# Performance work log

Measured on AMD Instinct MI355X. Metric: run time of the kernel, lower is better.

## Reference

```python
import math
import jax, jax.numpy as jnp
import numpy as np

L, NH, DF = 4, 4, 32  # num_layers, num_heads, head_dim (H=128)
EPS = 1e-5


def ln(x, g, b):
    m = x.mean(-1, keepdims=True)
    v = ((x - m) ** 2).mean(-1, keepdims=True)
    return (x - m) * jax.lax.rsqrt(v + EPS) * g + b


def mha(x, w_in, b_in, w_out, b_out):
    # torch nn.MultiheadAttention self-attention, batch_first, no mask
    B, S, H = x.shape
    q, k, v = jnp.split(x @ w_in + b_in, 3, axis=-1)
    q = q.reshape(B, S, NH, DF)
    k = k.reshape(B, S, NH, DF)
    v = v.reshape(B, S, NH, DF)
    s = jnp.einsum('bqhd,bkhd->bhqk', q, k) / math.sqrt(DF)
    a = jax.nn.softmax(s, axis=-1)
    o = jnp.einsum('bhqk,bkhd->bqhd', a, v).reshape(B, S, H)
    return o @ w_out + b_out


def _forward(X_k, time_embed, step_embed, W_tr, b_tr, W_in, b_in, g_in, be_in,
             W_e, b_e, aw, ab, ow, ob, tng, tnb, f1w, f1b, f2w, f2b, fng, fnb,
             Wq, Wk, Wv, Wo, bo, Wem, bem, Wea, bea, e1w, e1b, e2w, e2b,
             gng, gnb, eng, enb, W_out, b_out, k_index, edge_index):
    B, N, T1, Cin = X_k.shape
    H = W_in.shape[1]
    # --- precompute_graph: self-loops + structural edge features ---
    loop = jnp.arange(N, dtype=edge_index.dtype)
    ei = jnp.concatenate([edge_index, jnp.stack([loop, loop])], axis=1)
    dst, src = ei[0], ei[1]
    E = ei.shape[1]
    deg = jnp.zeros((N,), jnp.float32).at[dst].add(1.0)
    deg_max = jnp.maximum(deg.max(), 1.0)
    edge_w = 1.0 / jnp.maximum(deg[dst], 1.0)
    feat = jnp.stack([edge_w, deg[src] / deg_max, deg[dst] / deg_max], axis=1)  # [E,3]
    # --- input embedding ---
    t_emb = time_embed  # [T1, te] (lookup of arange(T1) = whole table)
    X = jnp.concatenate(
        [X_k, jnp.broadcast_to(t_emb[None, None], (B, N, T1, t_emb.shape[-1]))], axis=-1)
    h = ln(X @ W_in + b_in, g_in, be_in)
    h = h + step_embed[k_index][:, None, None, :]
    e = feat @ W_e + b_e                       # [E, de]
    t_re = t_emb @ W_tr + b_tr                 # [T1, H]
    BT = B * T1
    for l in range(L):
        # temporal attention over T1
        h_flat = h.reshape(B * N, T1, H)
        attn_out = mha(h_flat, aw[l], ab[l], ow[l], ob[l])
        h = ln(h + attn_out.reshape(B, N, T1, H), tng[l], tnb[l])
        ffn = jax.nn.gelu(h @ f1w[l] + f1b[l], approximate=False) @ f2w[l] + f2b[l]
        h = ln(h + ffn, fng[l], fnb[l])
        h = h + t_re[None, None]
        # DiGress GT sparse graph block over N
        h_BT = h.transpose(0, 2, 1, 3).reshape(BT, N, H)
        Q = (h_BT @ Wq[l]).reshape(BT, N, NH, DF)
        K = (h_BT @ Wk[l]).reshape(BT, N, NH, DF)
        V = (h_BT @ Wv[l]).reshape(BT, N, NH, DF)
        scores = (Q[:, dst] * K[:, src]).sum(-1) / math.sqrt(DF)  # [BT,E,NH]
        scores = scores * (e @ Wem[l] + bem[l] + 1.0) + (e @ Wea[l] + bea[l])
        s_max = jax.lax.stop_gradient(scores.max(axis=1, keepdims=True))
        exp_s = jnp.exp(scores - s_max)
        denom = jnp.zeros((BT, N, NH), exp_s.dtype).at[:, dst, :].add(exp_s)
        attn = exp_s / (denom[:, dst, :] + 1e-9)
        agg = (attn[..., None] * V[:, src]).reshape(BT, E, H)
        out = jnp.zeros((BT, N, H), h.dtype).at[:, dst, :].add(agg)
        h_BT = h_BT + out @ Wo[l] + bo[l]
        h_mean = jax.lax.stop_gradient(h_BT).mean(0)               # [N,H]
        e_in = jnp.concatenate([h_mean[dst], h_mean[src], e], axis=-1)
        e_mlp = jax.nn.gelu(e_in @ e1w[l] + e1b[l], approximate=False) @ e2w[l] + e2b[l]
        e = ln(e + e_mlp, eng[l], enb[l])
        h = ln(h_BT.reshape(B, T1, N, H).transpose(0, 2, 1, 3), gng[l], gnb[l])
    return jax.nn.softmax(h @ W_out + b_out, axis=-1)


def setup_inputs() -> dict:
    key = jax.random.key(0)
    B, N, T1 = 2, 2000, 12
    sd, cc, te, H, de, nh = 4, 2, 16, 128, 16, 4
    Cin = (1 + cc) * sd  # 12
    E0, max_steps = 32000, 1024
    ks = iter(jax.random.split(key, 60))
    def rn(*shape, s=0.05):
        return jax.random.normal(next(ks), shape, jnp.float32) * s
    z = lambda *s: jnp.zeros(s, jnp.float32)
    o = lambda *s: jnp.ones(s, jnp.float32)
    return dict(
        X_k=jax.random.normal(next(ks), (B, N, T1, Cin), jnp.float32),
        time_embed=rn(T1, te), step_embed=rn(max_steps, H),
        W_tr=rn(te, H), b_tr=z(H),
        W_in=rn(Cin + te, H), b_in=z(H), g_in=o(H), be_in=z(H),
        W_e=rn(3, de), b_e=z(de),
        aw=rn(L, H, 3 * H), ab=z(L, 3 * H), ow=rn(L, H, H), ob=z(L, H),
        tng=o(L, H), tnb=z(L, H),
        f1w=rn(L, H, 2 * H), f1b=z(L, 2 * H), f2w=rn(L, 2 * H, H), f2b=z(L, H),
        fng=o(L, H), fnb=z(L, H),
        Wq=rn(L, H, H), Wk=rn(L, H, H), Wv=rn(L, H, H),
        Wo=rn(L, H, H), bo=z(L, H),
        Wem=rn(L, de, nh), bem=z(L, nh), Wea=rn(L, de, nh), bea=z(L, nh),
        e1w=rn(L, 2 * H + de, 4 * de), e1b=z(L, 4 * de),
        e2w=rn(L, 4 * de, de), e2b=z(L, de),
        gng=o(L, H), gnb=z(L, H), eng=o(L, de), enb=z(L, de),
        W_out=rn(H, sd), b_out=z(sd),
        k_index=jax.random.randint(next(ks), (B,), 0, max_steps),
        edge_index=jax.random.randint(next(ks), (2, E0), 0, N),
    )


def reference(X_k, time_embed, step_embed, W_tr, b_tr, W_in, b_in, g_in, be_in,
              W_e, b_e, aw, ab, ow, ob, tng, tnb, f1w, f1b, f2w, f2b, fng, fnb,
              Wq, Wk, Wv, Wo, bo, Wem, bem, Wea, bea, e1w, e1b, e2w, e2b,
              gng, gnb, eng, enb, W_out, b_out, k_index, edge_index):
    return _forward(X_k, time_embed, step_embed, W_tr, b_tr, W_in, b_in, g_in, be_in,
                    W_e, b_e, aw, ab, ow, ob, tng, tnb, f1w, f1b, f2w, f2b, fng, fnb,
                    Wq, Wk, Wv, Wo, bo, Wem, bem, Wea, bea, e1w, e1b, e2w, e2b,
                    gng, gnb, eng, enb, W_out, b_out, k_index, edge_index)
```

## Files before the change

### kernel.cpp

```cpp
#include <hip/hip_runtime.h>
#include <math.h>

#define NN 2000
#define T1C 12
#define BBC 2
#define HHC 128
#define NHD 4
#define DFD 32
#define LLC 4
#define DEC 16
#define TEC 16
#define CINC 12
#define E0C 32000
#define EEC 34000
#define BTC 24
#define MROWS 48000
#define EPSLN 1e-5f
#define SCALEQK 0.17677669529663687f

typedef __attribute__((ext_vector_type(8))) short short8;
typedef __attribute__((ext_vector_type(4))) float f32x4;


__device__ __forceinline__ unsigned short f2b(float f)
{
    unsigned u = __float_as_uint(f);
    return (unsigned short)((u + 0x7FFF + ((u >> 16) & 1)) >> 16);
}

__device__ __forceinline__ float b2f(unsigned short h)
{
    return __uint_as_float(((unsigned)h) << 16);
}


__global__ __launch_bounds__(256) void convwp_k(const float* __restrict__ W, unsigned short* __restrict__ Bp,
                                                int LN_, int K, int N, int noff, int Ntot)
{
    int idx = blockIdx.x * blockDim.x + threadIdx.x;
    int total = LN_ * K * N;
    if (idx >= total) return;
    int l = idx / (K * N);
    int r = idx - l * (K * N);
    int k = r / N;
    int n = r - k * N + noff;
    size_t off = (size_t)l * K * Ntot +
                 ((size_t)((n >> 4) * (K >> 5) + (k >> 5)) << 9) +
                 (((k >> 3) & 3) << 7) + ((n & 15) << 3) + (k & 7);
    Bp[off] = f2b(W[idx]);
}

__global__ __launch_bounds__(256) void convw12_k(const float* __restrict__ e1w, unsigned short* __restrict__ W12P)
{
    int idx = blockIdx.x * blockDim.x + threadIdx.x;
    if (idx >= LLC * 128 * 128) return;
    int l = idx >> 14;
    int r = idx & 16383;
    int c = r >> 7, k = r & 127;
    int sk = (c < 64) ? k : k + 128;
    int sc = c & 63;
    W12P[idx] = f2b(e1w[((size_t)l * 272 + sk) * 64 + sc]);
}

__global__ __launch_bounds__(256) void convwoT_k(const float* __restrict__ Wo, unsigned short* __restrict__ WoT)
{
    int idx = blockIdx.x * blockDim.x + threadIdx.x;
    if (idx >= LLC * 128 * 128) return;
    int l = idx >> 14;
    int r = idx & 16383;
    int c = r >> 7, k = r & 127;
    WoT[idx] = f2b(Wo[((size_t)l * 128 + k) * 128 + c]);
}


template<int K, int EPI, int OUTM>
__global__ __launch_bounds__(256) void gemm2_k(
    const unsigned short* __restrict__ A, const unsigned short* __restrict__ Bp,
    const float* __restrict__ bias, float* __restrict__ C, unsigned short* __restrict__ Cb,
    const float* __restrict__ res, const float* __restrict__ gam, const float* __restrict__ bet,
    const float* __restrict__ trep,
    int M, int Ntot)
{
    __shared__ unsigned short A_s[128 * 16 * 8];
    __shared__ float red2[2][128][2];

    int tid = threadIdx.x;
    int w = tid >> 6, lane = tid & 63;
    int wr = w & 1, wc = w >> 1;
    int quad = lane >> 4, lr = lane & 15;

    const unsigned short* abase = A + (size_t)blockIdx.x * 128 * K;
    int ntg0 = blockIdx.y * 8 + wc * 4;

    f32x4 acc[4][4];
#pragma unroll
    for (int mt = 0; mt < 4; mt++)
#pragma unroll
        for (int nt = 0; nt < 4; nt++) acc[mt][nt] = (f32x4){0.f, 0.f, 0.f, 0.f};

#pragma unroll
    for (int kb = 0; kb < K; kb += 128) {
        if (kb) __syncthreads();
#pragma unroll
        for (int j = 0; j < 8; j++) {
            int s = j * 256 + tid;
            int row = s >> 4, ks = s & 15;
            int ko = ks ^ (row & 15);
            uint4 d = *(const uint4*)(abase + (size_t)row * K + kb + ko * 8);
            *(uint4*)(A_s + s * 8) = d;
        }
        __syncthreads();
#pragma unroll
        for (int k0 = 0; k0 < 128; k0 += 32) {
            short8 af[4], bf[4];
#pragma unroll
            for (int mt = 0; mt < 4; mt++) {
                int row_l = wr * 64 + mt * 16 + lr;
                int koct = (k0 >> 3) + quad;
                int slot = row_l * 16 + (koct ^ lr);
                af[mt] = *(const short8*)(A_s + slot * 8);
            }
#pragma unroll
            for (int nt = 0; nt < 4; nt++) {
                size_t off = ((size_t)(ntg0 + nt) * (K >> 5) + ((kb + k0) >> 5)) * 512 + lane * 8;
                bf[nt] = *(const short8*)(Bp + off);
            }
#pragma unroll
            for (int mt = 0; mt < 4; mt++)
#pragma unroll
                for (int nt = 0; nt < 4; nt++)
                    acc[mt][nt] = __builtin_amdgcn_mfma_f32_16x16x32_bf16(af[mt], bf[nt], acc[mt][nt], 0, 0, 0);
        }
    }

    int rbase = blockIdx.x * 128 + wr * 64;
    int cbase = blockIdx.y * 128 + wc * 64;

    if constexpr (EPI != 3 && EPI != 4 && EPI != 5) {
#pragma unroll
        for (int mt = 0; mt < 4; mt++) {
#pragma unroll
            for (int nt = 0; nt < 4; nt++) {
                int colg = cbase + nt * 16 + lr;
                float bv = bias ? bias[colg] : 0.f;
#pragma unroll
                for (int i = 0; i < 4; i++) {
                    int row = rbase + mt * 16 + quad * 4 + i;
                    float x = acc[mt][nt][i] + bv;
                    if constexpr (EPI == 1) x = 0.5f * x * (1.f + erff(x * 0.70710678118654752f));
                    if constexpr (EPI == 2) x = res[(size_t)row * Ntot + colg] + x;
                    if constexpr (OUTM & 1) C[(size_t)row * Ntot + colg] = x;
                    if constexpr (OUTM & 4)
                        Cb[(size_t)blockIdx.y * M * 128 + (size_t)row * 128 + (wc * 64 + nt * 16 + lr)] = f2b(x);
                    else if constexpr (OUTM & 2)
                        Cb[(size_t)row * Ntot + colg] = f2b(x);
                }
            }
        }
    } else {
        float s[4][4], s2l[4][4];
#pragma unroll
        for (int mt = 0; mt < 4; mt++)
#pragma unroll
            for (int i = 0; i < 4; i++) { s[mt][i] = 0.f; s2l[mt][i] = 0.f; }
#pragma unroll
        for (int mt = 0; mt < 4; mt++) {
#pragma unroll
            for (int nt = 0; nt < 4; nt++) {
                int colg = cbase + nt * 16 + lr;
                float bv = bias[colg];
#pragma unroll
                for (int i = 0; i < 4; i++) {
                    int row = rbase + mt * 16 + quad * 4 + i;
                    float x = acc[mt][nt][i] + bv + res[(size_t)row * 128 + colg];
                    acc[mt][nt][i] = x;
                    s[mt][i] += x;
                    s2l[mt][i] += x * x;
                }
            }
        }
#pragma unroll
        for (int m = 1; m < 16; m <<= 1) {
#pragma unroll
            for (int mt = 0; mt < 4; mt++)
#pragma unroll
                for (int i = 0; i < 4; i++) {
                    s[mt][i]  += __shfl_xor(s[mt][i], m, 64);
                    s2l[mt][i] += __shfl_xor(s2l[mt][i], m, 64);
                }
        }
        if (lr == 0) {
#pragma unroll
            for (int mt = 0; mt < 4; mt++)
#pragma unroll
                for (int i = 0; i < 4; i++) {
                    int rl = wr * 64 + mt * 16 + quad * 4 + i;
                    red2[wc][rl][0] = s[mt][i];
                    red2[wc][rl][1] = s2l[mt][i];
                }
        }
        __syncthreads();
#pragma unroll
        for (int mt = 0; mt < 4; mt++) {
#pragma unroll
            for (int i = 0; i < 4; i++) {
                int rl = wr * 64 + mt * 16 + quad * 4 + i;
                float st  = red2[0][rl][0] + red2[1][rl][0];
                float s2t = red2[0][rl][1] + red2[1][rl][1];
                float mu = st * (1.f / 128.f);
                float rstd = rsqrtf(s2t * (1.f / 128.f) - mu * mu + EPSLN);
                int row = rbase + mt * 16 + quad * 4 + i;
                if constexpr (EPI == 4) {
                    int t = row % T1C;
                    int bn = row / T1C;
                    int b = bn / NN;
                    int n = bn - b * NN;
                    size_t rowp = (size_t)(b * T1C + t) * NN + n;
                    const float* trow = trep + t * HHC;
#pragma unroll
                    for (int nt = 0; nt < 4; nt++) {
                        int colg = cbase + nt * 16 + lr;
                        float y = (acc[mt][nt][i] - mu) * rstd * gam[colg] + bet[colg] + trow[colg];
                        C[rowp * 128 + colg] = y;
                        Cb[rowp * 128 + colg] = f2b(y);
                    }
                } else if constexpr (EPI == 5) {
                    int bt = row / NN, n = row - bt * NN;
                    int b = bt / T1C, t = bt - b * T1C;
                    size_t rowp = ((size_t)(b * NN + n)) * T1C + t;
#pragma unroll
                    for (int nt = 0; nt < 4; nt++) {
                        int colg = cbase + nt * 16 + lr;
                        float y = (acc[mt][nt][i] - mu) * rstd * gam[colg] + bet[colg];
                        C[rowp * 128 + colg] = y;
                        Cb[rowp * 128 + colg] = f2b(y);
                    }
                } else {
#pragma unroll
                    for (int nt = 0; nt < 4; nt++) {
                        int colg = cbase + nt * 16 + lr;
                        float y = (acc[mt][nt][i] - mu) * rstd * gam[colg] + bet[colg];
                        if constexpr (OUTM & 1) C[(size_t)row * 128 + colg] = y;
                        if constexpr (OUTM & 2) Cb[(size_t)row * 128 + colg] = f2b(y);
                    }
                }
            }
        }
    }
}

template<int K, int EPI, int OUTM>
static void run_gemm2(const unsigned short* A, const unsigned short* Bp, const float* bias,
                      float* C, unsigned short* Cb, const float* res, const float* g, const float* be,
                      const float* trep, int M, int Ntot, hipStream_t stream)
{
    dim3 grid(M / 128, Ntot / 128);
    gemm2_k<K, EPI, OUTM><<<grid, 256, 0, stream>>>(A, Bp, bias, C, Cb, res, g, be, trep, M, Ntot);
}


__global__ __launch_bounds__(256) void offn_k(
    const unsigned short* __restrict__ A,
    const unsigned short* __restrict__ Wp,
    const float* __restrict__ ob_l,
    const float* __restrict__ resh,
    const float* __restrict__ tng_l, const float* __restrict__ tnb_l,
    const unsigned short* __restrict__ F1p,
    const unsigned short* __restrict__ F2p,
    const float* __restrict__ f1b_l, const float* __restrict__ f2b_l,
    const float* __restrict__ fng_l, const float* __restrict__ fnb_l,
    const float* __restrict__ trep,
    const unsigned short* __restrict__ Wqkv,
    float* __restrict__ C,
    unsigned short* __restrict__ Qc, unsigned short* __restrict__ Kc, unsigned short* __restrict__ Vc)
{
    __shared__ unsigned short A_s[32 * 16 * 8];
    __shared__ unsigned short M_s[32 * 16 * 8];
    __shared__ float red2[2][32][2];

    int tid = threadIdx.x;
    int w = tid >> 6, lane = tid & 63;
    int wr = w & 1, wc = w >> 1;
    int quad = lane >> 4, lr = lane & 15;

    const unsigned short* abase = A + (size_t)blockIdx.x * 32 * 128;

#pragma unroll
    for (int j = 0; j < 2; j++) {
        int s = j * 256 + tid;
        int row = s >> 4, ks = s & 15;
        int ko = ks ^ (row & 15);
        uint4 d = *(const uint4*)(abase + (size_t)row * 128 + ko * 8);
        *(uint4*)(A_s + s * 8) = d;
    }
    __syncthreads();

    f32x4 wacc[4];
#pragma unroll
    for (int nt = 0; nt < 4; nt++) wacc[nt] = (f32x4){0.f, 0.f, 0.f, 0.f};
#pragma unroll
    for (int k0 = 0; k0 < 128; k0 += 32) {
        int row_l = wr * 16 + lr;
        int koct = (k0 >> 3) + quad;
        int slot = row_l * 16 + (koct ^ lr);
        short8 af = *(const short8*)(A_s + slot * 8);
        short8 bf[4];
#pragma unroll
        for (int nt = 0; nt < 4; nt++) {
            size_t off = ((size_t)(wc * 4 + nt) * 4 + (k0 >> 5)) * 512 + lane * 8;
            bf[nt] = *(const short8*)(Wp + off);
        }
#pragma unroll
        for (int nt = 0; nt < 4; nt++)
            wacc[nt] = __builtin_amdgcn_mfma_f32_16x16x32_bf16(af, bf[nt], wacc[nt], 0, 0, 0);
    }

    int rbase = blockIdx.x * 32 + wr * 16;
    int cbase = wc * 64;

    float yv[4][4];
    {
        float s1[4], s2v[4];
#pragma unroll
        for (int i = 0; i < 4; i++) { s1[i] = 0.f; s2v[i] = 0.f; }
#pragma unroll
        for (int nt = 0; nt < 4; nt++) {
            int colg = cbase + nt * 16 + lr;
            float bv = ob_l[colg];
#pragma unroll
            for (int i = 0; i < 4; i++) {
                int row = rbase + quad * 4 + i;
                float x = wacc[nt][i] + bv + resh[(size_t)row * 128 + colg];
                yv[nt][i] = x;
                s1[i] += x;
                s2v[i] += x * x;
            }
        }
#pragma unroll
        for (int m = 1; m < 16; m <<= 1) {
#pragma unroll
            for (int i = 0; i < 4; i++) {
                s1[i]  += __shfl_xor(s1[i], m, 64);
                s2v[i] += __shfl_xor(s2v[i], m, 64);
            }
        }
        if (lr == 0) {
#pragma unroll
            for (int i = 0; i < 4; i++) {
                int rl = wr * 16 + quad * 4 + i;
                red2[wc][rl][0] = s1[i];
                red2[wc][rl][1] = s2v[i];
            }
        }
        __syncthreads();
#pragma unroll
        for (int i = 0; i < 4; i++) {
            int rl = wr * 16 + quad * 4 + i;
            float st  = red2[0][rl][0] + red2[1][rl][0];
            float s2t = red2[0][rl][1] + red2[1][rl][1];
            float mu = st * (1.f / 128.f);
            float rstd = rsqrtf(s2t * (1.f / 128.f) - mu * mu + EPSLN);
            int row = wr * 16 + quad * 4 + i;
#pragma unroll
            for (int nt = 0; nt < 4; nt++) {
                int col = cbase + nt * 16 + lr;
                float y = (yv[nt][i] - mu) * rstd * tng_l[col] + tnb_l[col];
                yv[nt][i] = y;
                int cchunk = col >> 3, celem = col & 7;
                int ks = cchunk ^ (row & 15);
                A_s[(row * 16 + ks) * 8 + celem] = f2b(y);
            }
        }
    }
    __syncthreads();

    f32x4 facc[4];
#pragma unroll
    for (int nt = 0; nt < 4; nt++) facc[nt] = (f32x4){0.f, 0.f, 0.f, 0.f};

#pragma unroll
    for (int half = 0; half < 2; half++) {
        f32x4 macc[4];
#pragma unroll
        for (int nt = 0; nt < 4; nt++) macc[nt] = (f32x4){0.f, 0.f, 0.f, 0.f};
#pragma unroll
        for (int k0 = 0; k0 < 128; k0 += 32) {
            int row_l = wr * 16 + lr;
            int koct = (k0 >> 3) + quad;
            int slot = row_l * 16 + (koct ^ lr);
            short8 af = *(const short8*)(A_s + slot * 8);
            short8 bf[4];
#pragma unroll
            for (int nt = 0; nt < 4; nt++) {
                size_t off = ((size_t)(half * 8 + wc * 4 + nt) * 4 + (k0 >> 5)) * 512 + lane * 8;
                bf[nt] = *(const short8*)(F1p + off);
            }
#pragma unroll
            for (int nt = 0; nt < 4; nt++)
                macc[nt] = __builtin_amdgcn_mfma_f32_16x16x32_bf16(af, bf[nt], macc[nt], 0, 0, 0);
        }
        if (half) __syncthreads();
#pragma unroll
        for (int nt = 0; nt < 4; nt++) {
            int col = wc * 64 + nt * 16 + lr;
            float bv = f1b_l[half * 128 + col];
            int cchunk = col >> 3, celem = col & 7;
#pragma unroll
            for (int i = 0; i < 4; i++) {
                int row = wr * 16 + quad * 4 + i;
                float x = macc[nt][i] + bv;
                x = 0.5f * x * (1.f + erff(x * 0.70710678118654752f));
                int ks = cchunk ^ (row & 15);
                M_s[(row * 16 + ks) * 8 + celem] = f2b(x);
            }
        }
        __syncthreads();
#pragma unroll
        for (int k0 = 0; k0 < 128; k0 += 32) {
            int row_l = wr * 16 + lr;
            int koct = (k0 >> 3) + quad;
            int slot = row_l * 16 + (koct ^ lr);
            short8 af = *(const short8*)(M_s + slot * 8);
            short8 bf[4];
#pragma unroll
            for (int nt = 0; nt < 4; nt++) {
                size_t off = ((size_t)(wc * 4 + nt) * 8 + ((half * 128 + k0) >> 5)) * 512 + lane * 8;
                bf[nt] = *(const short8*)(F2p + off);
            }
#pragma unroll
            for (int nt = 0; nt < 4; nt++)
                facc[nt] = __builtin_amdgcn_mfma_f32_16x16x32_bf16(af, bf[nt], facc[nt], 0, 0, 0);
        }
    }

    float s[4], s2l[4];
#pragma unroll
    for (int i = 0; i < 4; i++) { s[i] = 0.f; s2l[i] = 0.f; }
#pragma unroll
    for (int nt = 0; nt < 4; nt++) {
        int colg = cbase + nt * 16 + lr;
        float bv = f2b_l[colg];
#pragma unroll
        for (int i = 0; i < 4; i++) {
            float x = facc[nt][i] + bv + yv[nt][i];
            facc[nt][i] = x;
            s[i] += x;
            s2l[i] += x * x;
        }
    }
#pragma unroll
    for (int m = 1; m < 16; m <<= 1) {
#pragma unroll
        for (int i = 0; i < 4; i++) {
            s[i]  += __shfl_xor(s[i], m, 64);
            s2l[i] += __shfl_xor(s2l[i], m, 64);
        }
    }
    if (lr == 0) {
#pragma unroll
        for (int i = 0; i < 4; i++) {
            int rl = wr * 16 + quad * 4 + i;
            red2[wc][rl][0] = s[i];
            red2[wc][rl][1] = s2l[i];
        }
    }
    __syncthreads();
    size_t rowp4[4];
#pragma unroll
    for (int i = 0; i < 4; i++) {
        int rl = wr * 16 + quad * 4 + i;
        float st  = red2[0][rl][0] + red2[1][rl][0];
        float s2t = red2[0][rl][1] + red2[1][rl][1];
        float mu = st * (1.f / 128.f);
        float rstd = rsqrtf(s2t * (1.f / 128.f) - mu * mu + EPSLN);
        int row = rbase + quad * 4 + i;
        int t = row % T1C;
        int bn = row / T1C;
        int b = bn / NN;
        int n = bn - b * NN;
        size_t rowp = (size_t)(b * T1C + t) * NN + n;
        rowp4[i] = rowp;
        const float* trow = trep + t * HHC;
        int rloc = wr * 16 + quad * 4 + i;
#pragma unroll
        for (int nt = 0; nt < 4; nt++) {
            int colg = cbase + nt * 16 + lr;
            float y = (facc[nt][i] - mu) * rstd * fng_l[colg] + fnb_l[colg] + trow[colg];
            C[rowp * 128 + colg] = y;
            int cchunk = colg >> 3, celem = colg & 7;
            int ks = cchunk ^ (rloc & 15);
            A_s[(rloc * 16 + ks) * 8 + celem] = f2b(y);
        }
    }
    __syncthreads();

#pragma unroll
    for (int g3 = 0; g3 < 3; g3++) {
        f32x4 qacc[4];
#pragma unroll
        for (int nt = 0; nt < 4; nt++) qacc[nt] = (f32x4){0.f, 0.f, 0.f, 0.f};
#pragma unroll
        for (int k0 = 0; k0 < 128; k0 += 32) {
            int row_l = wr * 16 + lr;
            int koct = (k0 >> 3) + quad;
            int slot = row_l * 16 + (koct ^ lr);
            short8 af = *(const short8*)(A_s + slot * 8);
            short8 bf[4];
#pragma unroll
            for (int nt = 0; nt < 4; nt++) {
                size_t off = ((size_t)(wc * 12 + g3 * 4 + nt) * 4 + (k0 >> 5)) * 512 + lane * 8;
                bf[nt] = *(const short8*)(Wqkv + off);
            }
#pragma unroll
            for (int nt = 0; nt < 4; nt++)
                qacc[nt] = __builtin_amdgcn_mfma_f32_16x16x32_bf16(af, bf[nt], qacc[nt], 0, 0, 0);
        }
#pragma unroll
        for (int nt = 0; nt < 4; nt++) {
            int colg = wc * 192 + (g3 * 4 + nt) * 16 + lr;
            unsigned short* dstbuf;
            int col;
            if (colg < 128)      { dstbuf = Qc; col = colg; }
            else if (colg < 256) { dstbuf = Kc; col = colg - 128; }
            else                 { dstbuf = Vc; col = colg - 256; }
#pragma unroll
            for (int i = 0; i < 4; i++)
                dstbuf[rowp4[i] * 128 + col] = f2b(qacc[nt][i]);
        }
    }
}


__global__ __launch_bounds__(256) void gemm_hm12_k(
    const unsigned short* __restrict__ A,
    const unsigned short* __restrict__ WT,
    const float* __restrict__ mA, const float* __restrict__ bo,
    const unsigned short* __restrict__ W12,
    float* __restrict__ P12)
{
    __shared__ unsigned short A_s[32 * 16 * 8];
    const int M = NN, K = 128;
    int tid = threadIdx.x;
    int w = tid >> 6, lane = tid & 63;
    int wr = w & 1, wc = w >> 1;
    int r0 = blockIdx.x * 32 + wr * 16;
    int c0 = wc * 64;
    int lr = lane & 15, quad = lane >> 4;
    int kq = quad * 8;
    int arow = r0 + lr; if (arow >= M) arow = M - 1;
    const unsigned short* ap = A + (size_t)arow * K + kq;
    const unsigned short* wp = WT + (size_t)(c0 + lr) * K + kq;

    f32x4 acc[4];
#pragma unroll
    for (int t = 0; t < 4; t++) acc[t] = (f32x4){0.f, 0.f, 0.f, 0.f};
    for (int k0 = 0; k0 < K; k0 += 32) {
        short8 a = *(const short8*)(ap + k0);
#pragma unroll
        for (int t = 0; t < 4; t++) {
            short8 b = *(const short8*)(wp + (size_t)t * 16 * K + k0);
            acc[t] = __builtin_amdgcn_mfma_f32_16x16x32_bf16(a, b, acc[t], 0, 0, 0);
        }
    }
#pragma unroll
    for (int t = 0; t < 4; t++) {
        int col = c0 + t * 16 + lr;
        int cchunk = col >> 3, celem = col & 7;
#pragma unroll
        for (int i = 0; i < 4; i++) {
            int row = r0 + quad * 4 + i;
            int rr = row < M ? row : M - 1;
            float x = acc[t][i] + mA[(size_t)rr * 128 + col] + bo[col];
            int rloc = wr * 16 + quad * 4 + i;
            int ks = cchunk ^ (rloc & 15);
            A_s[(rloc * 16 + ks) * 8 + celem] = f2b(x);
        }
    }
    __syncthreads();

    f32x4 acc2[4];
#pragma unroll
    for (int t = 0; t < 4; t++) acc2[t] = (f32x4){0.f, 0.f, 0.f, 0.f};
    const unsigned short* wp2 = W12 + (size_t)(c0 + lr) * 128 + kq;
#pragma unroll
    for (int k0 = 0; k0 < 128; k0 += 32) {
        int row_l = wr * 16 + lr;
        int koct = (k0 >> 3) + quad;
        int slot = row_l * 16 + (koct ^ lr);
        short8 af = *(const short8*)(A_s + slot * 8);
#pragma unroll
        for (int t = 0; t < 4; t++) {
            short8 b = *(const short8*)(wp2 + (size_t)t * 16 * 128 + k0);
            acc2[t] = __builtin_amdgcn_mfma_f32_16x16x32_bf16(af, b, acc2[t], 0, 0, 0);
        }
    }
#pragma unroll
    for (int t = 0; t < 4; t++) {
        int col = c0 + t * 16 + lr;
#pragma unroll
        for (int i = 0; i < 4; i++) {
            int row = r0 + quad * 4 + i;
            if (row < M) P12[(size_t)row * 128 + col] = acc2[t][i];
        }
    }
}


__global__ __launch_bounds__(256) void emlp_k(const float* __restrict__ P12,
                                              const int* __restrict__ dst, const int* __restrict__ src,
                                              const float* __restrict__ e1wE, const float* __restrict__ e1b_l,
                                              const float* __restrict__ e2w_l, const float* __restrict__ e2b_l,
                                              const float* __restrict__ g, const float* __restrict__ be,
                                              float* __restrict__ e,
                                              const int* __restrict__ epos,
                                              const float* __restrict__ WemN, const float* __restrict__ bemN,
                                              const float* __restrict__ WeaN, const float* __restrict__ beaN,
                                              float* __restrict__ ec, int doEc)
{
    __shared__ float tl[4][64];
    int wv = threadIdx.x >> 6, l = threadIdx.x & 63;
    int r = blockIdx.x * 4 + wv;
    int d = dst[r], s = src[r];
    const float* ep = e + (size_t)r * DEC;
    float t = P12[(size_t)d * 128 + l] + P12[(size_t)s * 128 + 64 + l] + e1b_l[l];
#pragma unroll
    for (int k = 0; k < DEC; k++) t += ep[k] * e1wE[k * 64 + l];
    t = 0.5f * t * (1.f + erff(t * 0.70710678118654752f));
    tl[wv][l] = t;
    __syncthreads();
    int c = l & 15, kq = l >> 4;
    float p = 0.f;
#pragma unroll
    for (int j = 0; j < 16; j++) p += tl[wv][kq * 16 + j] * e2w_l[(kq * 16 + j) * 16 + c];
    p += __shfl_xor(p, 16, 64);
    p += __shfl_xor(p, 32, 64);
    float x = p + e2b_l[c] + ep[c];
    float s1 = x, s2 = x * x;
#pragma unroll
    for (int m = 1; m < 16; m <<= 1) {
        s1 += __shfl_xor(s1, m, 64);
        s2 += __shfl_xor(s2, m, 64);
    }
    float mu = s1 * (1.f / 16.f);
    float rstd = rsqrtf(s2 * (1.f / 16.f) - mu * mu + EPSLN);
    float y = (x - mu) * rstd * g[c] + be[c];
    if (l < 16) e[(size_t)r * DEC + c] = y;

    if (doEc) {
        int hh = l >> 4;
        float pem = y * WemN[c * NHD + hh];
        float pea = y * WeaN[c * NHD + hh];
#pragma unroll
        for (int m = 1; m < 16; m <<= 1) {
            pem += __shfl_xor(pem, m, 64);
            pea += __shfl_xor(pea, m, 64);
        }
        if (c == 0) {
            int pos = epos[r];
            ec[(size_t)pos * 8 + hh * 2]     = (pem + bemN[hh] + 1.f) * SCALEQK;
            ec[(size_t)pos * 8 + hh * 2 + 1] = pea + beaN[hh];
        }
    }
}


__global__ __launch_bounds__(256) void zero_deg_k(int* __restrict__ degi)
{
    int i = blockIdx.x * blockDim.x + threadIdx.x;
    if (i < NN) degi[i] = 0;
}

__global__ __launch_bounds__(256) void build_edges_k(const int* __restrict__ eidx,
                                                     int* __restrict__ dst, int* __restrict__ src,
                                                     int* __restrict__ degi)
{
    int e = blockIdx.x * blockDim.x + threadIdx.x;
    if (e >= EEC) return;
    int d, s;
    if (e < E0C) { d = eidx[e]; s = eidx[E0C + e]; }
    else { d = e - E0C; s = e - E0C; }
    dst[e] = d;
    src[e] = s;
    atomicAdd(&degi[d], 1);
}

__global__ __launch_bounds__(256) void scan_k(const int* __restrict__ degi, int* __restrict__ rowptr,
                                              int* __restrict__ cursor, float* __restrict__ degmaxf)
{
    __shared__ int ssum[256];
    __shared__ int smx[256];
    int tid = threadIdx.x;
    int vals[8];
    int s = 0, mx = 0;
    int base = tid * 8;
#pragma unroll
    for (int j = 0; j < 8; j++) {
        int idx = base + j;
        int v = (idx < NN) ? degi[idx] : 0;
        vals[j] = v; s += v; mx = max(mx, v);
    }
    ssum[tid] = s; smx[tid] = mx;
    __syncthreads();
    for (int off = 1; off < 256; off <<= 1) {
        int t = (tid >= off) ? ssum[tid - off] : 0;
        __syncthreads();
        ssum[tid] += t;
        __syncthreads();
    }
    for (int off = 128; off > 0; off >>= 1) {
        if (tid < off) smx[tid] = max(smx[tid], smx[tid + off]);
        __syncthreads();
    }
    if (tid == 0) *degmaxf = fmaxf((float)smx[0], 1.f);
    int running = ssum[tid] - s;
#pragma unroll
    for (int j = 0; j < 8; j++) {
        int idx = base + j;
        if (idx < NN) { rowptr[idx] = running; cursor[idx] = running; running += vals[j]; }
    }
    if (tid == 255) rowptr[NN] = ssum[255];
}

__global__ __launch_bounds__(256) void feat_k(const int* __restrict__ dst, const int* __restrict__ src,
                                              const int* __restrict__ degi, const float* __restrict__ degmaxf,
                                              int* __restrict__ cursor, int* __restrict__ srcCSR,
                                              int* __restrict__ epos,
                                              const float* __restrict__ We, const float* __restrict__ bE,
                                              float* __restrict__ e)
{
    int ei = blockIdx.x * blockDim.x + threadIdx.x;
    if (ei >= EEC) return;
    int d = dst[ei], s = src[ei];
    int pos = atomicAdd(&cursor[d], 1);
    srcCSR[pos] = s;
    epos[ei] = pos;
    float dm = *degmaxf;
    float degd = (float)degi[d], degs = (float)degi[s];
    float f0 = 1.f / fmaxf(degd, 1.f);
    float f1 = degs / dm, f2 = degd / dm;
#pragma unroll
    for (int c = 0; c < DEC; c++)
        e[ei * DEC + c] = bE[c] + f0 * We[c] + f1 * We[DEC + c] + f2 * We[2 * DEC + c];
}


__global__ __launch_bounds__(256) void embed_k(const float* __restrict__ Xk, const float* __restrict__ temb,
                                               const float* __restrict__ Win, const float* __restrict__ bin,
                                               const float* __restrict__ g, const float* __restrict__ be,
                                               const float* __restrict__ stepemb, const int* __restrict__ kidx,
                                               float* __restrict__ h, unsigned short* __restrict__ hb)
{
    int row = blockIdx.x * 4 + (threadIdx.x >> 6);
    int l = threadIdx.x & 63;
    int t = row % T1C;
    int bn = row / T1C;
    int b = bn / NN;
    const float* xk = Xk + (size_t)row * CINC;
    const float* tp = temb + t * TEC;
    float acc0 = bin[l], acc1 = bin[l + 64];
#pragma unroll
    for (int k = 0; k < CINC; k++) {
        float xv = xk[k];
        acc0 += xv * Win[k * HHC + l];
        acc1 += xv * Win[k * HHC + l + 64];
    }
#pragma unroll
    for (int k = 0; k < TEC; k++) {
        float xv = tp[k];
        acc0 += xv * Win[(CINC + k) * HHC + l];
        acc1 += xv * Win[(CINC + k) * HHC + l + 64];
    }
    float s = acc0 + acc1, s2 = acc0 * acc0 + acc1 * acc1;
#pragma unroll
    for (int m = 32; m >= 1; m >>= 1) {
        s  += __shfl_xor(s, m, 64);
        s2 += __shfl_xor(s2, m, 64);
    }
    float mu = s * (1.f / 128.f);
    float rstd = rsqrtf(s2 * (1.f / 128.f) - mu * mu + EPSLN);
    const float* se = stepemb + (size_t)kidx[b] * HHC;
    float v0 = (acc0 - mu) * rstd * g[l] + be[l] + se[l];
    float v1 = (acc1 - mu) * rstd * g[l + 64] + be[l + 64] + se[l + 64];
    size_t ob = (size_t)row * HHC;
    h[ob + l] = v0;
    h[ob + l + 64] = v1;
    hb[ob + l] = f2b(v0);
    hb[ob + l + 64] = f2b(v1);
}

__global__ __launch_bounds__(128) void tre_k(const float* __restrict__ temb, const float* __restrict__ Wtr,
                                             const float* __restrict__ btr, float* __restrict__ tre)
{
    int t = blockIdx.x, c = threadIdx.x;
    float acc = btr[c];
#pragma unroll
    for (int k = 0; k < TEC; k++) acc += temb[t * TEC + k] * Wtr[k * HHC + c];
    tre[t * HHC + c] = acc;
}


__global__ __launch_bounds__(128) void temporal_attn_k(const unsigned short* __restrict__ qkvb,
                                                       unsigned short* __restrict__ outb)
{
    int bn = blockIdx.x;
    __shared__ unsigned short qkv_s[T1C][408];
    __shared__ float s[NHD][T1C][T1C];
    int tid = threadIdx.x;
    int hh = tid >> 5, lane = tid & 31;
    const unsigned short* base = qkvb + (size_t)bn * T1C * 384;
    for (int cIdx = tid; cIdx < 576; cIdx += 128) {
        uint4 d = *(const uint4*)(base + cIdx * 8);
        int t = cIdx / 48;
        int c0 = (cIdx - t * 48) * 8;
        *(uint4*)(&qkv_s[t][c0]) = d;
    }
    __syncthreads();
    for (int idx = lane; idx < T1C * T1C; idx += 32) {
        int tq = idx / T1C, tk = idx - tq * T1C;
        const unsigned* qp = (const unsigned*)&qkv_s[tq][hh * 32];
        const unsigned* kp = (const unsigned*)&qkv_s[tk][128 + hh * 32];
        float acc = 0.f;
#pragma unroll
        for (int d = 0; d < 16; d++) {
            unsigned a = qp[d], b = kp[d];
            acc += __uint_as_float(a << 16) * __uint_as_float(b << 16);
            acc += __uint_as_float(a & 0xFFFF0000u) * __uint_as_float(b & 0xFFFF0000u);
        }
        s[hh][tq][tk] = acc * SCALEQK;
    }
    __syncthreads();
    if (tid < NHD * T1C) {
        int h2 = tid / T1C, tq = tid - h2 * T1C;
        float mx = -1e30f;
#pragma unroll
        for (int j = 0; j < T1C; j++) mx = fmaxf(mx, s[h2][tq][j]);
        float sum = 0.f;
#pragma unroll
        for (int j = 0; j < T1C; j++) { float ex = __expf(s[h2][tq][j] - mx); s[h2][tq][j] = ex; sum += ex; }
        float inv = 1.f / sum;
#pragma unroll
        for (int j = 0; j < T1C; j++) s[h2][tq][j] *= inv;
    }
    __syncthreads();
    int oc = hh * 32 + lane;
#pragma unroll
    for (int t = 0; t < T1C; t++) {
        float acc = 0.f;
#pragma unroll
        for (int tk = 0; tk < T1C; tk++) acc += s[hh][t][tk] * b2f(qkv_s[tk][256 + oc]);
        outb[((size_t)bn * T1C + t) * HHC + oc] = f2b(acc);
    }
}


__global__ __launch_bounds__(256) void emea_k(const float* __restrict__ e, const int* __restrict__ epos,
                                              const float* __restrict__ Wem, const float* __restrict__ bem,
                                              const float* __restrict__ Wea, const float* __restrict__ bea,
                                              float* __restrict__ ec)
{
    int r = blockIdx.x * blockDim.x + threadIdx.x;
    if (r >= EEC) return;
    float ev[DEC];
#pragma unroll
    for (int k = 0; k < DEC; k++) ev[k] = e[r * DEC + k];
    int pos = epos[r];
#pragma unroll
    for (int hh = 0; hh < NHD; hh++) {
        float a = bem[hh], b2 = bea[hh];
#pragma unroll
        for (int k = 0; k < DEC; k++) { a += ev[k] * Wem[k * NHD + hh]; b2 += ev[k] * Wea[k * NHD + hh]; }
        ec[(size_t)pos * 8 + hh * 2]     = (a + 1.f) * SCALEQK;
        ec[(size_t)pos * 8 + hh * 2 + 1] = b2;
    }
}

__global__ __launch_bounds__(256) void sagg_k(const unsigned short* __restrict__ Q,
                                              const unsigned short* __restrict__ K,
                                              const unsigned short* __restrict__ V,
                                              const int* __restrict__ rowptr, const int* __restrict__ srcCSR,
                                              const float* __restrict__ ec, unsigned short* __restrict__ outb)
{
    int wv = threadIdx.x >> 6;
    int lane = threadIdx.x & 63;
    int blk = blockIdx.x;
    int bt = blk % BTC;
    int n  = (blk / BTC) * 4 + wv;
    int cg = lane & 15;
    int es = lane >> 4;
    int hh = cg >> 2;
    size_t base = (size_t)bt * NN;
    uint4 qd = *(const uint4*)(Q + (base + n) * HHC + cg * 8);
    unsigned qv[4] = {qd.x, qd.y, qd.z, qd.w};
    float q[8];
#pragma unroll
    for (int jj = 0; jj < 4; jj++) {
        q[2 * jj]     = __uint_as_float(qv[jj] << 16);
        q[2 * jj + 1] = __uint_as_float(qv[jj] & 0xFFFF0000u);
    }
    int s0 = rowptr[n], s1 = rowptr[n + 1];
    float acc[8];
#pragma unroll
    for (int j = 0; j < 8; j++) acc[j] = 0.f;
    float den = 0.f;
    for (int i = s0 + es; i < s1; i += 4) {
        int sn = srcCSR[i];
        uint4 kd = *(const uint4*)(K + (base + sn) * HHC + cg * 8);
        uint4 vd = *(const uint4*)(V + (base + sn) * HHC + cg * 8);
        float2 c2 = *(const float2*)(ec + (size_t)i * 8 + hh * 2);
        unsigned kv[4] = {kd.x, kd.y, kd.z, kd.w};
        float p = 0.f;
#pragma unroll
        for (int jj = 0; jj < 4; jj++) {
            p += q[2 * jj]     * __uint_as_float(kv[jj] << 16);
            p += q[2 * jj + 1] * __uint_as_float(kv[jj] & 0xFFFF0000u);
        }
        p += __shfl_xor(p, 1, 64);
        p += __shfl_xor(p, 2, 64);
        float w = __expf(p * c2.x + c2.y);
        unsigned vv[4] = {vd.x, vd.y, vd.z, vd.w};
#pragma unroll
        for (int jj = 0; jj < 4; jj++) {
            acc[2 * jj]     += w * __uint_as_float(vv[jj] << 16);
            acc[2 * jj + 1] += w * __uint_as_float(vv[jj] & 0xFFFF0000u);
        }
        den += w;
    }
#pragma unroll
    for (int j = 0; j < 8; j++) {
        acc[j] += __shfl_xor(acc[j], 16, 64);
        acc[j] += __shfl_xor(acc[j], 32, 64);
    }
    den += __shfl_xor(den, 16, 64);
    den += __shfl_xor(den, 32, 64);
    if (es == 0) {
        float inv = den + 1e-9f;
        unsigned short r[8];
#pragma unroll
        for (int j = 0; j < 8; j++) r[j] = f2b(acc[j] / inv);
        *(uint4*)(outb + (base + n) * HHC + cg * 8) = *(uint4*)r;
    }
}

__global__ __launch_bounds__(128) void hmean2_k(const float* __restrict__ hBT,
                                                const unsigned short* __restrict__ aggb,
                                                float* __restrict__ mA, unsigned short* __restrict__ mBb)
{
    int n = blockIdx.x, c = threadIdx.x;
    float sA = 0.f, sB = 0.f;
#pragma unroll
    for (int bt = 0; bt < BTC; bt++) {
        size_t off = ((size_t)bt * NN + n) * HHC + c;
        sA += hBT[off];
        sB += b2f(aggb[off]);
    }
    mA[n * HHC + c] = sA * (1.f / BTC);
    mBb[n * HHC + c] = f2b(sB * (1.f / BTC));
}


__global__ __launch_bounds__(256) void out_k(const float* __restrict__ h, const float* __restrict__ Wout,
                                             const float* __restrict__ bout, float* __restrict__ out)
{
    int row = blockIdx.x * 4 + (threadIdx.x >> 6);
    int lane = threadIdx.x & 63;
    const float* hp = h + (size_t)row * HHC;
    float x0 = hp[lane], x1 = hp[lane + 64];
    float w00 = Wout[lane * 4 + 0], w01 = Wout[lane * 4 + 1];
    float w02 = Wout[lane * 4 + 2], w03 = Wout[lane * 4 + 3];
    float w10 = Wout[(lane + 64) * 4 + 0], w11 = Wout[(lane + 64) * 4 + 1];
    float w12 = Wout[(lane + 64) * 4 + 2], w13 = Wout[(lane + 64) * 4 + 3];
    float p0 = x0 * w00 + x1 * w10;
    float p1 = x0 * w01 + x1 * w11;
    float p2 = x0 * w02 + x1 * w12;
    float p3 = x0 * w03 + x1 * w13;
#pragma unroll
    for (int m = 32; m >= 1; m >>= 1) {
        p0 += __shfl_xor(p0, m, 64);
        p1 += __shfl_xor(p1, m, 64);
        p2 += __shfl_xor(p2, m, 64);
        p3 += __shfl_xor(p3, m, 64);
    }
    if (lane == 0) {
        float l0 = p0 + bout[0], l1 = p1 + bout[1], l2 = p2 + bout[2], l3 = p3 + bout[3];
        float mx = fmaxf(fmaxf(l0, l1), fmaxf(l2, l3));
        float e0 = __expf(l0 - mx), e1 = __expf(l1 - mx), e2 = __expf(l2 - mx), e3 = __expf(l3 - mx);
        float inv = 1.f / (e0 + e1 + e2 + e3);
        float4 o = {e0 * inv, e1 * inv, e2 * inv, e3 * inv};
        *(float4*)(out + (size_t)row * 4) = o;
    }
}


extern "C" void kernel_launch(void* const* d_in, const int* in_sizes, int n_in,
                              void* d_out, int out_size, void* d_ws, size_t ws_size,
                              hipStream_t stream)
{
    const float* Xk      = (const float*)d_in[0];
    const float* temb    = (const float*)d_in[1];
    const float* stepemb = (const float*)d_in[2];
    const float* Wtr     = (const float*)d_in[3];
    const float* btr     = (const float*)d_in[4];
    const float* Win     = (const float*)d_in[5];
    const float* bin     = (const float*)d_in[6];
    const float* gin     = (const float*)d_in[7];
    const float* bein    = (const float*)d_in[8];
    const float* We      = (const float*)d_in[9];
    const float* bE      = (const float*)d_in[10];
    const float* aw      = (const float*)d_in[11];
    const float* ab      = (const float*)d_in[12];
    const float* ow      = (const float*)d_in[13];
    const float* ob      = (const float*)d_in[14];
    const float* tng     = (const float*)d_in[15];
    const float* tnb     = (const float*)d_in[16];
    const float* f1w     = (const float*)d_in[17];
    const float* f1b     = (const float*)d_in[18];
    const float* f2w     = (const float*)d_in[19];
    const float* f2b_    = (const float*)d_in[20];
    const float* fng     = (const float*)d_in[21];
    const float* fnb     = (const float*)d_in[22];
    const float* Wq      = (const float*)d_in[23];
    const float* Wk      = (const float*)d_in[24];
    const float* Wv      = (const float*)d_in[25];
    const float* Wo      = (const float*)d_in[26];
    const float* bo      = (const float*)d_in[27];
    const float* Wem     = (const float*)d_in[28];
    const float* bem     = (const float*)d_in[29];
    const float* Wea     = (const float*)d_in[30];
    const float* bea     = (const float*)d_in[31];
    const float* e1w     = (const float*)d_in[32];
    const float* e1b     = (const float*)d_in[33];
    const float* e2w     = (const float*)d_in[34];
    const float* e2b     = (const float*)d_in[35];
    const float* gng     = (const float*)d_in[36];
    const float* gnb     = (const float*)d_in[37];
    const float* eng     = (const float*)d_in[38];
    const float* enb     = (const float*)d_in[39];
    const float* Wout    = (const float*)d_in[40];
    const float* bout    = (const float*)d_in[41];
    const int*   kidx    = (const int*)d_in[42];
    const int*   eidx    = (const int*)d_in[43];
    float* outp = (float*)d_out;

    char* wsp = (char*)d_ws;
    auto alloc = [&](size_t nbytes) -> void* {
        void* p = (void*)wsp;
        wsp += (nbytes + 255) & ~(size_t)255;
        return p;
    };
    float* h     = (float*)alloc((size_t)MROWS * HHC * 4);
    unsigned short* hb = (unsigned short*)alloc((size_t)MROWS * HHC * 2);
    float* hBT   = (float*)alloc((size_t)MROWS * HHC * 4);
    float* bufC  = (float*)alloc((size_t)MROWS * 384 * 4);
    unsigned short* bufDb = (unsigned short*)alloc((size_t)MROWS * HHC * 2);
    float* ebuf  = (float*)alloc((size_t)EEC * DEC * 4);
    float* ec    = (float*)alloc((size_t)EEC * NHD * 2 * 4);
    float* P12   = (float*)alloc((size_t)NN * HHC * 4);
    float* mA    = (float*)alloc((size_t)NN * HHC * 4);
    unsigned short* mBb = (unsigned short*)alloc((size_t)NN * HHC * 2);
    float* tre   = (float*)alloc((size_t)T1C * HHC * 4);
    float* degmaxf = (float*)alloc(4);
    int* degi   = (int*)alloc((size_t)NN * 4);
    int* dst    = (int*)alloc((size_t)EEC * 4);
    int* srcA   = (int*)alloc((size_t)EEC * 4);
    int* srcCSR = (int*)alloc((size_t)EEC * 4);
    int* epos   = (int*)alloc((size_t)EEC * 4);
    int* rowptr = (int*)alloc((size_t)(NN + 1) * 4);
    int* cursor = (int*)alloc((size_t)NN * 4);
    unsigned short* awP   = (unsigned short*)alloc((size_t)LLC * 384 * 128 * 2);
    unsigned short* owP   = (unsigned short*)alloc((size_t)LLC * 128 * 128 * 2);
    unsigned short* f1P   = (unsigned short*)alloc((size_t)LLC * 256 * 128 * 2);
    unsigned short* f2P   = (unsigned short*)alloc((size_t)LLC * 128 * 256 * 2);
    unsigned short* WqkvP = (unsigned short*)alloc((size_t)LLC * 384 * 128 * 2);
    unsigned short* WoP   = (unsigned short*)alloc((size_t)LLC * 128 * 128 * 2);
    unsigned short* WoT   = (unsigned short*)alloc((size_t)LLC * 128 * 128 * 2);
    unsigned short* W12P  = (unsigned short*)alloc((size_t)LLC * 128 * 128 * 2);

    unsigned short* bufCb = (unsigned short*)bufC;
    unsigned short* Qc    = (unsigned short*)bufC;
    unsigned short* Kc    = Qc + (size_t)MROWS * HHC;
    unsigned short* Vc    = Kc + (size_t)MROWS * HHC;

    {
        auto cwp = [&](const float* W, unsigned short* Bp, int K, int N, int noff, int Ntot) {
            int total = LLC * K * N;
            convwp_k<<<(total + 255) / 256, 256, 0, stream>>>(W, Bp, LLC, K, N, noff, Ntot);
        };
        cwp(aw,  awP, 128, 384, 0, 384);
        cwp(ow,  owP, 128, 128, 0, 128);
        cwp(f1w, f1P, 128, 256, 0, 256);
        cwp(f2w, f2P, 256, 128, 0, 128);
        cwp(Wq,  WqkvP, 128, 128, 0,   384);
        cwp(Wk,  WqkvP, 128, 128, 128, 384);
        cwp(Wv,  WqkvP, 128, 128, 256, 384);
        cwp(Wo,  WoP, 128, 128, 0, 128);
        convwoT_k<<<(LLC * 128 * 128 + 255) / 256, 256, 0, stream>>>(Wo, WoT);
        convw12_k<<<(LLC * 128 * 128 + 255) / 256, 256, 0, stream>>>(e1w, W12P);
    }

    zero_deg_k<<<(NN + 255) / 256, 256, 0, stream>>>(degi);
    build_edges_k<<<(EEC + 255) / 256, 256, 0, stream>>>(eidx, dst, srcA, degi);
    scan_k<<<1, 256, 0, stream>>>(degi, rowptr, cursor, degmaxf);
    feat_k<<<(EEC + 255) / 256, 256, 0, stream>>>(dst, srcA, degi, degmaxf, cursor, srcCSR, epos, We, bE, ebuf);

    embed_k<<<MROWS / 4, 256, 0, stream>>>(Xk, temb, Win, bin, gin, bein, stepemb, kidx, h, hb);
    tre_k<<<T1C, 128, 0, stream>>>(temb, Wtr, btr, tre);

    emea_k<<<(EEC + 255) / 256, 256, 0, stream>>>(ebuf, epos, Wem, bem, Wea, bea, ec);

    for (int l = 0; l < LLC; l++) {
        const unsigned short* awP_l   = awP   + (size_t)l * 384 * 128;
        const unsigned short* owP_l   = owP   + (size_t)l * 128 * 128;
        const unsigned short* f1P_l   = f1P   + (size_t)l * 256 * 128;
        const unsigned short* f2P_l   = f2P   + (size_t)l * 128 * 256;
        const unsigned short* WqkvP_l = WqkvP + (size_t)l * 384 * 128;
        const unsigned short* WoP_l   = WoP   + (size_t)l * 128 * 128;
        const unsigned short* WoT_l   = WoT   + (size_t)l * 128 * 128;
        const unsigned short* W12P_l  = W12P  + (size_t)l * 128 * 128;
        const float* ab_l  = ab  + (size_t)l * 3 * HHC;
        const float* ob_l  = ob  + (size_t)l * HHC;
        const float* tng_l = tng + (size_t)l * HHC;
        const float* tnb_l = tnb + (size_t)l * HHC;
        const float* f1b_l = f1b + (size_t)l * 256;
        const float* f2b_l = f2b_ + (size_t)l * HHC;
        const float* fng_l = fng + (size_t)l * HHC;
        const float* fnb_l = fnb + (size_t)l * HHC;
        const float* bo_l  = bo  + (size_t)l * HHC;
        const float* e1wE_l = e1w + ((size_t)l * 272 + 256) * 64;
        const float* e1b_l = e1b + (size_t)l * 64;
        const float* e2w_l = e2w + (size_t)l * 64 * DEC;
        const float* e2b_l = e2b + (size_t)l * DEC;
        const float* gng_l = gng + (size_t)l * HHC;
        const float* gnb_l = gnb + (size_t)l * HHC;
        const float* eng_l = eng + (size_t)l * DEC;
        const float* enb_l = enb + (size_t)l * DEC;
        int ln = (l + 1 < LLC) ? l + 1 : l;
        const float* WemN = Wem + (size_t)ln * DEC * NHD;
        const float* bemN = bem + (size_t)ln * NHD;
        const float* WeaN = Wea + (size_t)ln * DEC * NHD;
        const float* beaN = bea + (size_t)ln * NHD;
        int doEc = (l + 1 < LLC) ? 1 : 0;

        run_gemm2<128, 0, 2>(hb, awP_l, ab_l, nullptr, bufCb, nullptr, nullptr, nullptr, nullptr, MROWS, 384, stream);
        temporal_attn_k<<<BBC * NN, 128, 0, stream>>>(bufCb, bufDb);
        offn_k<<<MROWS / 32, 256, 0, stream>>>(bufDb, owP_l, ob_l, h, tng_l, tnb_l,
                                               f1P_l, f2P_l, f1b_l, f2b_l, fng_l, fnb_l,
                                               tre, WqkvP_l, hBT, Qc, Kc, Vc);
        sagg_k<<<BTC * (NN / 4), 256, 0, stream>>>(Qc, Kc, Vc, rowptr, srcCSR, ec, bufDb);
        hmean2_k<<<NN, 128, 0, stream>>>(hBT, bufDb, mA, mBb);
        run_gemm2<128, 5, 3>(bufDb, WoP_l, bo_l, h, hb, hBT, gng_l, gnb_l, nullptr, MROWS, 128, stream);
        gemm_hm12_k<<<(NN + 31) / 32, 256, 0, stream>>>(mBb, WoT_l, mA, bo_l, W12P_l, P12);
        emlp_k<<<EEC / 4, 256, 0, stream>>>(P12, dst, srcA, e1wE_l, e1b_l, e2w_l, e2b_l, eng_l, enb_l, ebuf,
                                            epos, WemN, bemN, WeaN, beaN, ec, doEc);
    }

    out_k<<<MROWS / 4, 256, 0, stream>>>(h, Wout, bout, outp);
}
```

Measured before the change: 933.3 us.

## Fuse next layer's QKV projection into the LayerNorm epilogue of the output GEMM

The spatial output GEMM with its LayerNorm epilogue now also keeps the normalized bf16 tile in shared memory and runs the next layer's QKV projection on it, writing Q/K/V straight into bufCb in permuted row order. The standalone QKV GEMM in each layer is removed, except for a single launch before the loop for layer 0. This drops one kernel launch per layer and the write and re-read of the bf16 hidden copy (hb). In exchange the fused kernel does three times more MFMA work per block while its grid stays at 375 blocks, which may serialise work that used to be spread over 1125 blocks.

```diff
diff --git a/kernel.cpp b/kernel.cpp
--- a/kernel.cpp
+++ b/kernel.cpp
@@ -73,16 +73,19 @@
 }
 
 
-template<int K, int EPI, int OUTM>
+template<int K, int EPI, int OUTM, int QKV>
 __global__ __launch_bounds__(256) void gemm2_k(
     const unsigned short* __restrict__ A, const unsigned short* __restrict__ Bp,
     const float* __restrict__ bias, float* __restrict__ C, unsigned short* __restrict__ Cb,
     const float* __restrict__ res, const float* __restrict__ gam, const float* __restrict__ bet,
     const float* __restrict__ trep,
+    const unsigned short* __restrict__ Wqkv, const float* __restrict__ abq,
+    unsigned short* __restrict__ outQ,
     int M, int Ntot)
 {
     __shared__ unsigned short A_s[128 * 16 * 8];
     __shared__ float red2[2][128][2];
+    __shared__ int rowp_s[128];
 
     int tid = threadIdx.x;
     int w = tid >> 6, lane = tid & 63;
@@ -136,7 +139,7 @@
     int rbase = blockIdx.x * 128 + wr * 64;
     int cbase = blockIdx.y * 128 + wc * 64;
 
-    if constexpr (EPI != 3 && EPI != 4 && EPI != 5) {
+    if constexpr (EPI != 3 && EPI != 5) {
 #pragma unroll
         for (int mt = 0; mt < 4; mt++) {
 #pragma unroll
@@ -150,10 +153,7 @@
                     if constexpr (EPI == 1) x = 0.5f * x * (1.f + erff(x * 0.70710678118654752f));
                     if constexpr (EPI == 2) x = res[(size_t)row * Ntot + colg] + x;
                     if constexpr (OUTM & 1) C[(size_t)row * Ntot + colg] = x;
-                    if constexpr (OUTM & 4)
-                        Cb[(size_t)blockIdx.y * M * 128 + (size_t)row * 128 + (wc * 64 + nt * 16 + lr)] = f2b(x);
-                    else if constexpr (OUTM & 2)
-                        Cb[(size_t)row * Ntot + colg] = f2b(x);
+                    if constexpr (OUTM & 2) Cb[(size_t)row * Ntot + colg] = f2b(x);
                 }
             }
         }
@@ -210,30 +210,22 @@
                 float mu = st * (1.f / 128.f);
                 float rstd = rsqrtf(s2t * (1.f / 128.f) - mu * mu + EPSLN);
                 int row = rbase + mt * 16 + quad * 4 + i;
-                if constexpr (EPI == 4) {
-                    int t = row % T1C;
-                    int bn = row / T1C;
-                    int b = bn / NN;
-                    int n = bn - b * NN;
-                    size_t rowp = (size_t)(b * T1C + t) * NN + n;
-                    const float* trow = trep + t * HHC;
-#pragma unroll
-                    for (int nt = 0; nt < 4; nt++) {
-                        int colg = cbase + nt * 16 + lr;
-                        float y = (acc[mt][nt][i] - mu) * rstd * gam[colg] + bet[colg] + trow[colg];
-                        C[rowp * 128 + colg] = y;
-                        Cb[rowp * 128 + colg] = f2b(y);
-                    }
-                } else if constexpr (EPI == 5) {
+                if constexpr (EPI == 5) {
                     int bt = row / NN, n = row - bt * NN;
                     int b = bt / T1C, t = bt - b * T1C;
                     size_t rowp = ((size_t)(b * NN + n)) * T1C + t;
+                    if (QKV && lr == 0) rowp_s[rl] = (int)rowp;
 #pragma unroll
                     for (int nt = 0; nt < 4; nt++) {
                         int colg = cbase + nt * 16 + lr;
                         float y = (acc[mt][nt][i] - mu) * rstd * gam[colg] + bet[colg];
                         C[rowp * 128 + colg] = y;
-                        Cb[rowp * 128 + colg] = f2b(y);
+                        if constexpr (OUTM & 2) Cb[rowp * 128 + colg] = f2b(y);
+                        if constexpr (QKV) {
+                            int cchunk = colg >> 3, celem = colg & 7;
+                            int ks = cchunk ^ (rl & 15);
+                            A_s[(rl * 16 + ks) * 8 + celem] = f2b(y);
+                        }
                     }
                 } else {
 #pragma unroll
@@ -247,6 +239,52 @@
             }
         }
     }
+
+    if constexpr (QKV) {
+        __syncthreads();
+#pragma unroll
+        for (int g3 = 0; g3 < 3; g3++) {
+            f32x4 qacc[4][4];
+#pragma unroll
+            for (int mt = 0; mt < 4; mt++)
+#pragma unroll
+                for (int nt = 0; nt < 4; nt++) qacc[mt][nt] = (f32x4){0.f, 0.f, 0.f, 0.f};
+#pragma unroll
+            for (int k0 = 0; k0 < 128; k0 += 32) {
+                short8 af[4], bf[4];
+#pragma unroll
+                for (int mt = 0; mt < 4; mt++) {
+                    int row_l = wr * 64 + mt * 16 + lr;
+                    int koct = (k0 >> 3) + quad;
+                    int slot = row_l * 16 + (koct ^ lr);
+                    af[mt] = *(const short8*)(A_s + slot * 8);
+                }
+#pragma unroll
+                for (int nt = 0; nt < 4; nt++) {
+                    size_t off = ((size_t)(wc * 12 + g3 * 4 + nt) * 4 + (k0 >> 5)) * 512 + lane * 8;
+                    bf[nt] = *(const short8*)(Wqkv + off);
+                }
+#pragma unroll
+                for (int mt = 0; mt < 4; mt++)
+#pragma unroll
+                    for (int nt = 0; nt < 4; nt++)
+                        qacc[mt][nt] = __builtin_amdgcn_mfma_f32_16x16x32_bf16(af[mt], bf[nt], qacc[mt][nt], 0, 0, 0);
+            }
+#pragma unroll
+            for (int nt = 0; nt < 4; nt++) {
+                int col = (wc * 12 + g3 * 4 + nt) * 16 + lr;
+                float bv = abq[col];
+#pragma unroll
+                for (int mt = 0; mt < 4; mt++) {
+#pragma unroll
+                    for (int i = 0; i < 4; i++) {
+                        int row = rowp_s[wr * 64 + mt * 16 + quad * 4 + i];
+                        outQ[(size_t)row * 384 + col] = f2b(qacc[mt][nt][i] + bv);
+                    }
+                }
+            }
+        }
+    }
 }
 
 template<int K, int EPI, int OUTM>
@@ -255,7 +293,19 @@
                       const float* trep, int M, int Ntot, hipStream_t stream)
 {
     dim3 grid(M / 128, Ntot / 128);
-    gemm2_k<K, EPI, OUTM><<<grid, 256, 0, stream>>>(A, Bp, bias, C, Cb, res, g, be, trep, M, Ntot);
+    gemm2_k<K, EPI, OUTM, 0><<<grid, 256, 0, stream>>>(A, Bp, bias, C, Cb, res, g, be, trep,
+                                                       nullptr, nullptr, nullptr, M, Ntot);
+}
+
+template<int QKV>
+static void run_gemm2_ln_qkv(const unsigned short* A, const unsigned short* Bp, const float* bias,
+                             float* C, const float* res, const float* g, const float* be,
+                             const unsigned short* Wqkv, const float* abq, unsigned short* outQ,
+                             hipStream_t stream)
+{
+    dim3 grid(MROWS / 128, 1);
+    gemm2_k<128, 5, 1, QKV><<<grid, 256, 0, stream>>>(A, Bp, bias, C, nullptr, res, g, be, nullptr,
+                                                      Wqkv, abq, outQ, MROWS, 128);
 }
 
 
@@ -1107,8 +1157,9 @@
 
     emea_k<<<(EEC + 255) / 256, 256, 0, stream>>>(ebuf, epos, Wem, bem, Wea, bea, ec);
 
+    run_gemm2<128, 0, 2>(hb, awP, ab, nullptr, bufCb, nullptr, nullptr, nullptr, nullptr, MROWS, 384, stream);
+
     for (int l = 0; l < LLC; l++) {
-        const unsigned short* awP_l   = awP   + (size_t)l * 384 * 128;
         const unsigned short* owP_l   = owP   + (size_t)l * 128 * 128;
         const unsigned short* f1P_l   = f1P   + (size_t)l * 256 * 128;
         const unsigned short* f2P_l   = f2P   + (size_t)l * 128 * 256;
@@ -1116,7 +1167,6 @@
         const unsigned short* WoP_l   = WoP   + (size_t)l * 128 * 128;
         const unsigned short* WoT_l   = WoT   + (size_t)l * 128 * 128;
         const unsigned short* W12P_l  = W12P  + (size_t)l * 128 * 128;
-        const float* ab_l  = ab  + (size_t)l * 3 * HHC;
         const float* ob_l  = ob  + (size_t)l * HHC;
         const float* tng_l = tng + (size_t)l * HHC;
         const float* tnb_l = tnb + (size_t)l * HHC;
@@ -1139,15 +1189,19 @@
         const float* WeaN = Wea + (size_t)ln * DEC * NHD;
         const float* beaN = bea + (size_t)ln * NHD;
         int doEc = (l + 1 < LLC) ? 1 : 0;
-
-        run_gemm2<128, 0, 2>(hb, awP_l, ab_l, nullptr, bufCb, nullptr, nullptr, nullptr, nullptr, MROWS, 384, stream);
+        const unsigned short* awP_n = awP + (size_t)ln * 384 * 128;
+        const float* ab_n = ab + (size_t)ln * 3 * HHC;
+
         temporal_attn_k<<<BBC * NN, 128, 0, stream>>>(bufCb, bufDb);
         offn_k<<<MROWS / 32, 256, 0, stream>>>(bufDb, owP_l, ob_l, h, tng_l, tnb_l,
                                                f1P_l, f2P_l, f1b_l, f2b_l, fng_l, fnb_l,
                                                tre, WqkvP_l, hBT, Qc, Kc, Vc);
         sagg_k<<<BTC * (NN / 4), 256, 0, stream>>>(Qc, Kc, Vc, rowptr, srcCSR, ec, bufDb);
         hmean2_k<<<NN, 128, 0, stream>>>(hBT, bufDb, mA, mBb);
-        run_gemm2<128, 5, 3>(bufDb, WoP_l, bo_l, h, hb, hBT, gng_l, gnb_l, nullptr, MROWS, 128, stream);
+        if (l + 1 < LLC)
+            run_gemm2_ln_qkv<1>(bufDb, WoP_l, bo_l, h, hBT, gng_l, gnb_l, awP_n, ab_n, bufCb, stream);
+        else
+            run_gemm2_ln_qkv<0>(bufDb, WoP_l, bo_l, h, hBT, gng_l, gnb_l, nullptr, nullptr, nullptr, stream);
         gemm_hm12_k<<<(NN + 31) / 32, 256, 0, stream>>>(mBb, WoT_l, mA, bo_l, W12P_l, P12);
         emlp_k<<<EEC / 4, 256, 0, stream>>>(P12, dst, srcA, e1wE_l, e1b_l, e2w_l, e2b_l, eng_l, enb_l, ebuf,
                                             epos, WemN, bemN, WeaN, beaN, ec, doEc);
```

After: 961.1 us. 1.03x slower.
